# Kernel tuning notes

Hardware: AMD Instinct MI355X
Metric: run time of the kernel (lower is better)

## Reference

```python
import jax, jax.numpy as jnp
import numpy as np

B = 262144          # flattened batch of (sample, time) points
D = 16              # input_dim: number of independent per-dimension MLPs
TE = 3              # time_embedding_dim -> per-dim MLP input width = 1 + TE = 4
H = 64              # hidden width (model_dims = [64, 64, 1])


def setup_inputs() -> dict:
    key = jax.random.key(0)
    ks = jax.random.split(key, 8)
    s1 = 1.0 / np.sqrt(1 + TE)   # torch nn.Linear default init scale ~ U(-1/sqrt(fan_in), ...)
    s2 = 1.0 / np.sqrt(H)
    return {
        "t": jax.random.normal(ks[0], (B, TE), jnp.float32),
        "y": jax.random.normal(ks[1], (B, D), jnp.float32),
        # stacked per-dim weights: layer l weight [D, in_l, out_l], bias [D, out_l]
        "W1": jax.random.uniform(ks[2], (D, 1 + TE, H), jnp.float32, -s1, s1),
        "b1": jax.random.uniform(ks[3], (D, H), jnp.float32, -s1, s1),
        "W2": jax.random.uniform(ks[4], (D, H, H), jnp.float32, -s2, s2),
        "b2": jax.random.uniform(ks[5], (D, H), jnp.float32, -s2, s2),
        "W3": jax.random.uniform(ks[6], (D, H, 1), jnp.float32, -s2, s2),
        "b3": jax.random.uniform(ks[7], (D, 1), jnp.float32, -s2, s2),
    }


def reference(t, y, W1, b1, W2, b2, W3, b3):
    # Per-dim MLP input: concat([y_i, t]) -> [B, D, 1+TE]
    Bn, Dn = y.shape
    x = jnp.concatenate(
        [y[:, :, None], jnp.broadcast_to(t[:, None, :], (Bn, Dn, t.shape[-1]))], axis=-1
    )
    h = jax.nn.softplus(jnp.einsum("bdi,dih->bdh", x, W1) + b1)      # Linear + Softplus
    h = jax.nn.softplus(jnp.einsum("bdh,dhk->bdk", h, W2) + b2)      # Linear + Softplus
    out = jnp.einsum("bdk,dko->bdo", h, W3) + b3                      # final Linear, out=1
    # concat over D then final activation: [B, D]
    return jax.nn.softplus(out[..., 0])
```

## Files before the change

kernel.cpp:

```cpp
#include <hip/hip_runtime.h>
#include <cmath>

#define B_TOTAL 262144
#define D 16
#define TE 3
#define H 64

#define TILES_PER_BLOCK 16
#define FLUSH_GROUP 4
#define NBLOCKS (B_TOTAL / 16 / TILES_PER_BLOCK)

#define LOG2E 1.44269504088896340736f
#define LN2   0.693147180559945309417f

#define RS 68

typedef _Float16 half8  __attribute__((ext_vector_type(8)));
typedef __fp16   fp16x2 __attribute__((ext_vector_type(2)));
typedef float    f32x4  __attribute__((ext_vector_type(4)));
typedef unsigned int uint32;

__device__ __forceinline__ float sp_log2(float xs) {
    return __builtin_amdgcn_logf(1.0f + __builtin_amdgcn_exp2f(xs));
}
__device__ __forceinline__ float softplus_full(float x) {
    float e = __builtin_amdgcn_exp2f(-fabsf(x) * LOG2E);
    return fmaxf(x, 0.0f) + LN2 * __builtin_amdgcn_logf(1.0f + e);
}

__device__ __forceinline__ half8 pack8(const f32x4 f0, const f32x4 f1) {
    union { half8 h; fp16x2 p[4]; } a;
    a.p[0] = __builtin_amdgcn_cvt_pkrtz(f0.x, f0.y);
    a.p[1] = __builtin_amdgcn_cvt_pkrtz(f0.z, f0.w);
    a.p[2] = __builtin_amdgcn_cvt_pkrtz(f1.x, f1.y);
    a.p[3] = __builtin_amdgcn_cvt_pkrtz(f1.z, f1.w);
    return a.h;
}

__global__ __launch_bounds__(1024, 4) void DiagonalVariance_kernel(
    const float* __restrict__ t,
    const float* __restrict__ y,
    const float* __restrict__ W1,
    const float* __restrict__ b1,
    const float* __restrict__ W2,
    const float* __restrict__ b2,
    const float* __restrict__ W3,
    const float* __restrict__ b3,
    float* __restrict__ out)
{
    __shared__ __align__(16) float tbuf[D * 16 * RS];
    __shared__ float obuf[FLUSH_GROUP * 256];

    const int wave = threadIdx.x >> 6;
    const int lane = threadIdx.x & 63;
    const int q    = lane >> 4;
    const int lm   = lane & 15;
    const int d    = wave;
    const bool q0  = (q == 0);

    const float* __restrict__ W1d = W1 + d * (4 * H);
    const float* __restrict__ b1d = b1 + d * H;
    const float* __restrict__ W2d = W2 + d * (H * H);
    const float* __restrict__ b2d = b2 + d * H;
    const float* __restrict__ W3d = W3 + d * H;

    half8 w2f[2][4];
    #pragma unroll
    for (int ks = 0; ks < 2; ++ks)
        #pragma unroll
        for (int nt = 0; nt < 4; ++nt)
            #pragma unroll
            for (int j = 0; j < 8; ++j)
                w2f[ks][nt][j] = (_Float16)W2d[(32 * ks + 8 * q + j) * H + 16 * nt + lm];

    half8 w1f[4];
    #pragma unroll
    for (int nt = 0; nt < 4; ++nt) {
        #pragma unroll
        for (int j = 0; j < 8; ++j) {
            const int h = 16 * nt + lm;
            float v = 0.0f;
            if (q0 && j < 4)  v = W1d[j * H + h] * LOG2E;
            if (q0 && j == 4) v = b1d[h] * LOG2E;
            w1f[nt][j] = (_Float16)v;
        }
    }

    half8 w3f[2];
    #pragma unroll
    for (int ks = 0; ks < 2; ++ks)
        #pragma unroll
        for (int j = 0; j < 8; ++j)
            w3f[ks][j] = (_Float16)(W3d[32 * ks + 8 * q + j] * LN2);

    f32x4 b2f[4];
    #pragma unroll
    for (int nt = 0; nt < 4; ++nt) {
        const float bv = b2d[16 * nt + lm] * LOG2E;
        b2f[nt] = (f32x4){bv, bv, bv, bv};
    }
    const float b3v = b3[d];

    float* const tb  = tbuf + wave * (16 * RS);
    float* const twr = tb + (q * 4) * RS + lm;
    const float* const trd = tb + lm * RS + 8 * q;

    #pragma unroll 1
    for (int g = 0; g < TILES_PER_BLOCK / FLUSH_GROUP; ++g) {
        #pragma unroll 1
        for (int tg = 0; tg < FLUSH_GROUP; ++tg) {
            const int tile = blockIdx.x * TILES_PER_BLOCK + g * FLUSH_GROUP + tg;
            const int row  = tile * 16 + lm;

            const float x0 = y[row * D + d];
            const float t0 = t[row * TE + 0];
            const float t1 = t[row * TE + 1];
            const float t2 = t[row * TE + 2];
            union { half8 h; fp16x2 p[4]; uint32 u[4]; } af;
            const fp16x2 p0 = __builtin_amdgcn_cvt_pkrtz(x0, t0);
            const fp16x2 p1 = __builtin_amdgcn_cvt_pkrtz(t1, t2);
            af.u[0] = q0 ? __builtin_bit_cast(uint32, p0) : 0u;
            af.u[1] = q0 ? __builtin_bit_cast(uint32, p1) : 0u;
            af.u[2] = q0 ? 0x00003C00u : 0u;
            af.u[3] = 0u;

            f32x4 acc1[4];
            #pragma unroll
            for (int nt = 0; nt < 4; ++nt)
                acc1[nt] = __builtin_amdgcn_mfma_f32_16x16x32_f16(
                    af.h, w1f[nt], (f32x4){0.f, 0.f, 0.f, 0.f}, 0, 0, 0);

            #pragma unroll
            for (int nt = 0; nt < 4; ++nt)
                #pragma unroll
                for (int r = 0; r < 4; ++r)
                    twr[r * RS + nt * 16] = sp_log2(acc1[nt][r]);

            half8 a2[2];
            #pragma unroll
            for (int ks = 0; ks < 2; ++ks) {
                const f32x4 f0 = *(const f32x4*)(trd + 32 * ks);
                const f32x4 f1 = *(const f32x4*)(trd + 32 * ks + 4);
                a2[ks] = pack8(f0, f1);
            }

            f32x4 acc2[4];
            #pragma unroll
            for (int nt = 0; nt < 4; ++nt)
                acc2[nt] = __builtin_amdgcn_mfma_f32_16x16x32_f16(a2[0], w2f[0][nt], b2f[nt], 0, 0, 0);
            #pragma unroll
            for (int nt = 0; nt < 4; ++nt)
                acc2[nt] = __builtin_amdgcn_mfma_f32_16x16x32_f16(a2[1], w2f[1][nt], acc2[nt], 0, 0, 0);

            #pragma unroll
            for (int nt = 0; nt < 4; ++nt)
                #pragma unroll
                for (int r = 0; r < 4; ++r)
                    twr[r * RS + nt * 16] = sp_log2(acc2[nt][r]);

            half8 a3[2];
            #pragma unroll
            for (int ks = 0; ks < 2; ++ks) {
                const f32x4 f0 = *(const f32x4*)(trd + 32 * ks);
                const f32x4 f1 = *(const f32x4*)(trd + 32 * ks + 4);
                a3[ks] = pack8(f0, f1);
            }

            f32x4 acc3;
            acc3 = __builtin_amdgcn_mfma_f32_16x16x32_f16(a3[0], w3f[0], (f32x4){0.f, 0.f, 0.f, 0.f}, 0, 0, 0);
            acc3 = __builtin_amdgcn_mfma_f32_16x16x32_f16(a3[1], w3f[1], acc3, 0, 0, 0);

            const float v01 = (lm & 1) ? acc3[1] : acc3[0];
            const float v23 = (lm & 1) ? acc3[3] : acc3[2];
            const float vs  = (lm & 2) ? v23 : v01;
            if (lm < 4)
                obuf[tg * 256 + (q * 4 + lm) * D + d] = softplus_full(vs + b3v);
        }

        __syncthreads();
        out[blockIdx.x * (TILES_PER_BLOCK * 256) + g * 1024 + threadIdx.x] = obuf[threadIdx.x];
        __syncthreads();
    }
}

extern "C" void kernel_launch(void* const* d_in, const int* in_sizes, int n_in,
                              void* d_out, int out_size, void* d_ws, size_t ws_size,
                              hipStream_t stream) {
    const float* t  = (const float*)d_in[0];
    const float* y  = (const float*)d_in[1];
    const float* W1 = (const float*)d_in[2];
    const float* b1 = (const float*)d_in[3];
    const float* W2 = (const float*)d_in[4];
    const float* b2 = (const float*)d_in[5];
    const float* W3 = (const float*)d_in[6];
    const float* b3 = (const float*)d_in[7];
    float* out = (float*)d_out;

    DiagonalVariance_kernel<<<dim3(NBLOCKS), dim3(1024), 0, stream>>>(
        t, y, W1, b1, W2, b2, W3, b3, out);
}
```

Baseline: 228.3 us.

## Store hidden activations as fp16 in LDS and double-buffer output staging

The per-wave LDS transpose buffer now holds fp16 instead of fp32, so MFMA A-operands load directly as half8 with no per-element packing conversions, and LDS traffic and footprint are halved. The output staging buffer is double-buffered, which removes the second barrier per flush group. The q0 masking on the layer-1 input is also dropped: all quads now load real data where previously they were zeroed. Whether this is still correct depends on the W1 fragment zeroing the unused k positions, and the new row stride may change LDS bank conflicts.

```diff
diff --git a/kernel.cpp b/kernel.cpp
--- a/kernel.cpp
+++ b/kernel.cpp
@@ -13,7 +13,7 @@
 #define LOG2E 1.44269504088896340736f
 #define LN2   0.693147180559945309417f
 
-#define RS 68
+#define RSH 72
 
 typedef _Float16 half8  __attribute__((ext_vector_type(8)));
 typedef __fp16   fp16x2 __attribute__((ext_vector_type(2)));
@@ -28,15 +28,6 @@
     return fmaxf(x, 0.0f) + LN2 * __builtin_amdgcn_logf(1.0f + e);
 }
 
-__device__ __forceinline__ half8 pack8(const f32x4 f0, const f32x4 f1) {
-    union { half8 h; fp16x2 p[4]; } a;
-    a.p[0] = __builtin_amdgcn_cvt_pkrtz(f0.x, f0.y);
-    a.p[1] = __builtin_amdgcn_cvt_pkrtz(f0.z, f0.w);
-    a.p[2] = __builtin_amdgcn_cvt_pkrtz(f1.x, f1.y);
-    a.p[3] = __builtin_amdgcn_cvt_pkrtz(f1.z, f1.w);
-    return a.h;
-}
-
 __global__ __launch_bounds__(1024, 4) void DiagonalVariance_kernel(
     const float* __restrict__ t,
     const float* __restrict__ y,
@@ -48,8 +39,8 @@
     const float* __restrict__ b3,
     float* __restrict__ out)
 {
-    __shared__ __align__(16) float tbuf[D * 16 * RS];
-    __shared__ float obuf[FLUSH_GROUP * 256];
+    __shared__ __align__(16) _Float16 tbuf[D * 16 * RSH];
+    __shared__ float obuf[2][FLUSH_GROUP * 256];
 
     const int wave = threadIdx.x >> 6;
     const int lane = threadIdx.x & 63;
@@ -101,27 +92,27 @@
     }
     const float b3v = b3[d];
 
-    float* const tb  = tbuf + wave * (16 * RS);
-    float* const twr = tb + (q * 4) * RS + lm;
-    const float* const trd = tb + lm * RS + 8 * q;
+    _Float16* const tb  = tbuf + wave * (16 * RSH);
+    _Float16* const twr = tb + (q * 4) * RSH + lm;
+    const _Float16* const trd = tb + lm * RSH + 8 * q;
 
     #pragma unroll 1
     for (int g = 0; g < TILES_PER_BLOCK / FLUSH_GROUP; ++g) {
+        float* const ob = obuf[g & 1];
         #pragma unroll 1
         for (int tg = 0; tg < FLUSH_GROUP; ++tg) {
             const int tile = blockIdx.x * TILES_PER_BLOCK + g * FLUSH_GROUP + tg;
             const int row  = tile * 16 + lm;
 
+            const float* tp = t + row * TE;
             const float x0 = y[row * D + d];
-            const float t0 = t[row * TE + 0];
-            const float t1 = t[row * TE + 1];
-            const float t2 = t[row * TE + 2];
+            const float t0 = tp[0];
+            const float t1 = tp[1];
+            const float t2 = tp[2];
             union { half8 h; fp16x2 p[4]; uint32 u[4]; } af;
-            const fp16x2 p0 = __builtin_amdgcn_cvt_pkrtz(x0, t0);
-            const fp16x2 p1 = __builtin_amdgcn_cvt_pkrtz(t1, t2);
-            af.u[0] = q0 ? __builtin_bit_cast(uint32, p0) : 0u;
-            af.u[1] = q0 ? __builtin_bit_cast(uint32, p1) : 0u;
-            af.u[2] = q0 ? 0x00003C00u : 0u;
+            af.p[0] = __builtin_amdgcn_cvt_pkrtz(x0, t0);
+            af.p[1] = __builtin_amdgcn_cvt_pkrtz(t1, t2);
+            af.u[2] = 0x00003C00u;
             af.u[3] = 0u;
 
             f32x4 acc1[4];
@@ -134,15 +125,12 @@
             for (int nt = 0; nt < 4; ++nt)
                 #pragma unroll
                 for (int r = 0; r < 4; ++r)
-                    twr[r * RS + nt * 16] = sp_log2(acc1[nt][r]);
+                    twr[r * RSH + nt * 16] = (_Float16)sp_log2(acc1[nt][r]);
 
             half8 a2[2];
             #pragma unroll
-            for (int ks = 0; ks < 2; ++ks) {
-                const f32x4 f0 = *(const f32x4*)(trd + 32 * ks);
-                const f32x4 f1 = *(const f32x4*)(trd + 32 * ks + 4);
-                a2[ks] = pack8(f0, f1);
-            }
+            for (int ks = 0; ks < 2; ++ks)
+                a2[ks] = *(const half8*)(trd + 32 * ks);
 
             f32x4 acc2[4];
             #pragma unroll
@@ -156,15 +144,12 @@
             for (int nt = 0; nt < 4; ++nt)
                 #pragma unroll
                 for (int r = 0; r < 4; ++r)
-                    twr[r * RS + nt * 16] = sp_log2(acc2[nt][r]);
+                    twr[r * RSH + nt * 16] = (_Float16)sp_log2(acc2[nt][r]);
 
             half8 a3[2];
             #pragma unroll
-            for (int ks = 0; ks < 2; ++ks) {
-                const f32x4 f0 = *(const f32x4*)(trd + 32 * ks);
-                const f32x4 f1 = *(const f32x4*)(trd + 32 * ks + 4);
-                a3[ks] = pack8(f0, f1);
-            }
+            for (int ks = 0; ks < 2; ++ks)
+                a3[ks] = *(const half8*)(trd + 32 * ks);
 
             f32x4 acc3;
             acc3 = __builtin_amdgcn_mfma_f32_16x16x32_f16(a3[0], w3f[0], (f32x4){0.f, 0.f, 0.f, 0.f}, 0, 0, 0);
@@ -174,12 +159,11 @@
             const float v23 = (lm & 1) ? acc3[3] : acc3[2];
             const float vs  = (lm & 2) ? v23 : v01;
             if (lm < 4)
-                obuf[tg * 256 + (q * 4 + lm) * D + d] = softplus_full(vs + b3v);
+                ob[tg * 256 + (q * 4 + lm) * D + d] = softplus_full(vs + b3v);
         }
 
         __syncthreads();
-        out[blockIdx.x * (TILES_PER_BLOCK * 256) + g * 1024 + threadIdx.x] = obuf[threadIdx.x];
-        __syncthreads();
+        out[blockIdx.x * (TILES_PER_BLOCK * 256) + g * 1024 + threadIdx.x] = ob[threadIdx.x];
     }
 }
 
```

Result: slower. 233.2 us (+2.2%).
